# Optimization experiments

Measured on AMD Instinct MI355X. Metric: run time of the kernel, lower is better.

## Reference

```python
import jax, jax.numpy as jnp
import numpy as np

B, T, C = 16, 1024, 1024
H = 4          # wshare
K = 31         # kernel_size


def setup_inputs() -> dict:
    key = jax.random.key(0)
    ks = jax.random.split(key, 8)
    s = 1.0 / np.sqrt(C)
    return {
        "query": jax.random.normal(ks[0], (B, T, C), jnp.float32),
        "key_t": jax.random.normal(ks[1], (B, T, C), jnp.float32),   # unused, API compat
        "value": jax.random.normal(ks[2], (B, T, C), jnp.float32),   # unused, API compat
        "mask": jnp.ones((B, 1, T), jnp.int32),
        "W1": jax.random.uniform(ks[3], (2 * C, C), jnp.float32, -s, s),
        "b1": jnp.zeros((2 * C,), jnp.float32),
        "W2": jax.random.uniform(ks[4], (C, C), jnp.float32, -s, s),
        "b2": jnp.zeros((C,), jnp.float32),
        "conv_w": jax.random.uniform(ks[5], (H, K), jnp.float32, 0.0, 1.0),
        "bias": jnp.zeros((C,), jnp.float32),
    }


def reference(query, key_t, value, mask, W1, b1, W2, b2, conv_w, bias):
    # linear1 + GLU: (B,T,C) -> (B,T,2C) -> (B,T,C)
    x = query @ W1.T + b1
    a, g = jnp.split(x, 2, axis=-1)
    x = a * jax.nn.sigmoid(g)
    # (B,T,C) -> (B,C,T) -> (B*C/H, H, T); channel c uses shared kernel c % H
    x = jnp.transpose(x, (0, 2, 1)).reshape(B * C // H, H, T)
    # softmax-normalized shared kernels (H,K); dropout_rate=0 (eval)
    w = jax.nn.softmax(conv_w, axis=-1)
    y = jax.lax.conv_general_dilated(
        x, w[:, None, :], window_strides=(1,), padding=[(K // 2, K // 2)],
        feature_group_count=H, dimension_numbers=("NCH", "OIH", "NCH"))
    x = y.reshape(B, C, T) + bias[None, :, None]
    x = jnp.transpose(x, (0, 2, 1))               # (B,T,C)
    # padding mask: (B,1,T) -> transpose(-1,-2) -> (B,T,1), zero masked frames
    m = jnp.transpose(mask, (0, 2, 1))
    x = jnp.where(m == 0, 0.0, x)
    return x @ W2.T + b2
```

## Files before the change

### kernel.cpp

```cpp
#include <hip/hip_runtime.h>

typedef __attribute__((ext_vector_type(8))) __bf16 bf16x8;
typedef __attribute__((ext_vector_type(4))) __bf16 bf16x4;
typedef __attribute__((ext_vector_type(4))) float  f32x4;
typedef __attribute__((ext_vector_type(4))) float  float4v;

#define DEV static __device__ __forceinline__

DEV void gload_lds16(const void* g, void* l) {
  __builtin_amdgcn_global_load_lds(
      (const __attribute__((address_space(1))) void*)g,
      (__attribute__((address_space(3))) void*)l, 16, 0, 0);
}

__global__ void cvt_bf16_kernel(const float* __restrict__ in,
                                __bf16* __restrict__ out, int n4) {
  int stride = gridDim.x * blockDim.x;
  for (int i = blockIdx.x * blockDim.x + threadIdx.x; i < n4; i += stride) {
    float4v v = ((const float4v*)in)[i];
    bf16x4 o;
#pragma unroll
    for (int j = 0; j < 4; ++j) o[j] = (__bf16)v[j];
    ((bf16x4*)out)[i] = o;
  }
}

__global__ void softmax_w_kernel(const float* __restrict__ cw,
                                 float* __restrict__ out) {
  int h = threadIdx.x;
  if (h < 4) {
    float m = cw[h * 31];
#pragma unroll
    for (int k = 1; k < 31; ++k) m = fmaxf(m, cw[h * 31 + k]);
    float e[31];
    float s = 0.f;
#pragma unroll
    for (int k = 0; k < 31; ++k) {
      e[k] = __expf(cw[h * 31 + k] - m);
      s += e[k];
    }
    float inv = 1.f / s;
#pragma unroll
    for (int k = 0; k < 31; ++k) out[h * 31 + k] = e[k] * inv;
  }
}

template <int STORE_BF16>
__global__ __launch_bounds__(512, 2)
void gemm256_kernel(const __bf16* __restrict__ A, const __bf16* __restrict__ Bw,
                    const float* __restrict__ bias, void* __restrict__ Cout,
                    int M, int N, int K, int ntn) {
  __shared__ __align__(16) __bf16 Al[4 * 8192];
  __shared__ __align__(16) __bf16 Bl[4 * 8192];

  const int tid  = threadIdx.x;
  const int lane = tid & 63;
  const int w    = tid >> 6;
  const int wm = w >> 2, wn = w & 3;

  const int nwg = gridDim.x;
  const int cpx = nwg >> 3;
  const int bid = blockIdx.x;
  const int wgid = (bid & 7) * cpx + (bid >> 3);
  const int m0 = (wgid / ntn) * 256;
  const int n0 = (wgid % ntn) * 256;

  const int NT = K >> 6;

  const int srow = lane >> 2;
  const int scol = ((lane & 3) * 8) ^ (((lane >> 5) & 1) * 16);
  const __bf16* __restrict__ Abase = A + (long)m0 * K;
  const __bf16* __restrict__ Bbase = Bw + (long)n0 * K;

  const int l15 = lane & 15;
  const int cb  = ((lane >> 4) * 16) ^ (((lane >> 3) & 1) * 32);
  const int aoff = (wm * 128 + l15) * 64 + cb;
  const int boff = (wn * 64 + l15) * 64 + cb;

  f32x4 acc[8][4];
#pragma unroll
  for (int i = 0; i < 8; ++i)
#pragma unroll
    for (int j = 0; j < 4; ++j) {
      acc[i][j][0] = 0.f; acc[i][j][1] = 0.f;
      acc[i][j][2] = 0.f; acc[i][j][3] = 0.f;
    }
  bf16x8 af[8], bf[4];

#define ADST(c, s) (Al + ((c) * 2 + (s)) * 8192)
#define BDST(c, s) (Bl + ((c) * 2 + (s)) * 8192)
#define AGB(c, s) ((const char*)Al + ((c) * 2 + (s)) * 16384)
#define BGB(c, s) ((const char*)Bl + ((c) * 2 + (s)) * 16384)

#define STAGE(base, ktc, dst)                                               \
  {                                                                         \
    const __bf16* _src = (base) + (long)(w * 16 + srow) * K + (ktc) + scol; \
    gload_lds16(_src, (dst) + w * 512);                                     \
    gload_lds16(_src + (long)128 * K, (dst) + 4096 + w * 512);              \
  }

#define PH_MID()                                          \
  __builtin_amdgcn_s_barrier();                           \
  asm volatile("s_waitcnt lgkmcnt(0)" ::: "memory");      \
  __builtin_amdgcn_sched_barrier(0);                      \
  __builtin_amdgcn_s_setprio(1);

#define PH_END(VM)                                          \
  __builtin_amdgcn_s_setprio(0);                            \
  if (VM) asm volatile("s_waitcnt vmcnt(8)" ::: "memory");  \
  __builtin_amdgcn_s_barrier();

#define RD_A03(G)                                                  \
  _Pragma("unroll") for (int i = 0; i < 4; ++i)                    \
      af[i] = *(const bf16x8*)((G) + aoff + i * 1024);
#define RD_A47(G)                                                  \
  _Pragma("unroll") for (int i = 0; i < 4; ++i)                    \
      af[4 + i] = *(const bf16x8*)((G) + aoff + (4 + i) * 1024);
#define RD_B4(G)                                                   \
  _Pragma("unroll") for (int j = 0; j < 4; ++j)                    \
      bf[j] = *(const bf16x8*)((G) + boff + j * 1024);

#define MM03()                                                                 \
  _Pragma("unroll") for (int i = 0; i < 4; ++i)                                \
  _Pragma("unroll") for (int j = 0; j < 4; ++j)                                \
      acc[i][j] = __builtin_amdgcn_mfma_f32_16x16x32_bf16(af[i], bf[j], acc[i][j], 0, 0, 0);
#define MM47()                                                                 \
  _Pragma("unroll") for (int i = 0; i < 4; ++i)                                \
  _Pragma("unroll") for (int j = 0; j < 4; ++j)                                \
      acc[4 + i][j] = __builtin_amdgcn_mfma_f32_16x16x32_bf16(af[4 + i], bf[j], acc[4 + i][j], 0, 0, 0);

  STAGE(Abase, 0, ADST(0, 0));
  STAGE(Bbase, 0, BDST(0, 0));
  STAGE(Abase, 32, ADST(0, 1));
  STAGE(Bbase, 32, BDST(0, 1));
  STAGE(Abase, 64, ADST(1, 0));
  STAGE(Bbase, 64, BDST(1, 0));
  asm volatile("s_waitcnt vmcnt(8)" ::: "memory");
  __builtin_amdgcn_s_barrier();

#define TILE(tt, CUR)                                                \
  {                                                                  \
    const int k1 = (((tt) + 1 < NT) ? (tt) + 1 : NT - 1) * 64 + 32;  \
    const int k2 = (((tt) + 2 < NT) ? (tt) + 2 : NT - 1) * 64;       \
                                                            \
    RD_A03(AGB(CUR, 0)); RD_B4(BGB(CUR, 0));                         \
    STAGE(Abase, k1, ADST(CUR ^ 1, 1));                              \
    PH_MID(); MM03(); PH_END(0);                                     \
                                                            \
    RD_A47(AGB(CUR, 0));                                             \
    STAGE(Bbase, k1, BDST(CUR ^ 1, 1));                              \
    PH_MID(); MM47(); PH_END(1);                                     \
                                                            \
    RD_A03(AGB(CUR, 1)); RD_B4(BGB(CUR, 1));                         \
    STAGE(Abase, k2, ADST(CUR, 0));                                  \
    PH_MID(); MM03(); PH_END(0);                                     \
                                                            \
    RD_A47(AGB(CUR, 1));                                             \
    STAGE(Bbase, k2, BDST(CUR, 0));                                  \
    PH_MID(); MM47(); PH_END(1);                                     \
  }

#pragma unroll 1
  for (int t2 = 0; t2 < NT; t2 += 2) {
    TILE(t2, 0);
    TILE(t2 + 1, 1);
  }

  asm volatile("s_waitcnt vmcnt(0)" ::: "memory");

  const int crow = (lane >> 4) * 4;
  const int ccol = lane & 15;
#pragma unroll
  for (int i = 0; i < 8; ++i) {
#pragma unroll
    for (int j = 0; j < 4; ++j) {
      const int mrow = m0 + wm * 128 + i * 16 + crow;
      const int ncol = n0 + wn * 64 + j * 16 + ccol;
      const float bv = bias[ncol];
#pragma unroll
      for (int r = 0; r < 4; ++r) {
        float v = acc[i][j][r] + bv;
        if (STORE_BF16)
          ((__bf16*)Cout)[(long)(mrow + r) * N + ncol] = (__bf16)v;
        else
          ((float*)Cout)[(long)(mrow + r) * N + ncol] = v;
      }
    }
  }
#undef TILE
#undef STAGE
#undef PH_MID
#undef PH_END
#undef RD_A03
#undef RD_A47
#undef RD_B4
#undef MM03
#undef MM47
#undef ADST
#undef BDST
#undef AGB
#undef BGB
}

__global__ __launch_bounds__(256, 2)
void glu_conv_kernel(const __bf16* __restrict__ X, const float* __restrict__ Wsm,
                     const float* __restrict__ bias, const int* __restrict__ mask,
                     __bf16* __restrict__ Y) {
  const int b  = blockIdx.z;
  const int t0 = blockIdx.y * 64;
  const int c0 = blockIdx.x * 128;
  __shared__ float sgT[128][128];
  __shared__ float swl[124];
  const int tid = threadIdx.x;
  if (tid < 124) swl[tid] = Wsm[tid];

  for (int i = tid; i < 2048; i += 256) {
    const int ttl = i & 127;
    const int cg  = i >> 7;
    if (ttl < 94) {
      const int t = t0 - 15 + ttl;
      float v[8];
      if (t >= 0 && t < 1024) {
        const __bf16* p = X + ((long)(b * 1024 + t)) * 2048 + c0 + cg * 8;
        bf16x8 a8 = *(const bf16x8*)p;
        bf16x8 g8 = *(const bf16x8*)(p + 1024);
#pragma unroll
        for (int j = 0; j < 8; ++j) {
          float av = (float)a8[j], gv = (float)g8[j];
          v[j] = av / (1.f + __expf(-gv));
        }
      } else {
#pragma unroll
        for (int j = 0; j < 8; ++j) v[j] = 0.f;
      }
      const int q = ttl >> 2, e = ttl & 3;
#pragma unroll
      for (int j = 0; j < 8; ++j) {
        const int c = cg * 8 + j;
        sgT[c][((q ^ ((c & 7) << 2)) << 2) + e] = v[j];
      }
    }
  }
  __syncthreads();

  const int cc = tid & 127;
  const int th = tid >> 7;
  const int c  = c0 + cc;
  const float* wrow = swl + (c & 3) * 31;
  const float bv = bias[c];
  float acc[32];
#pragma unroll
  for (int u = 0; u < 32; ++u) acc[u] = bv;
  const int key = (cc & 7) << 2;
#pragma unroll
  for (int qi = 0; qi < 16; ++qi) {
    const int q = th * 8 + qi;
    const f32x4 w4 = *(const f32x4*)&sgT[cc][(q ^ key) << 2];
#pragma unroll
    for (int j = 0; j < 4; ++j) {
      const int rl = qi * 4 + j;
#pragma unroll
      for (int u = 0; u < 32; ++u) {
        const int k = rl - u;
        if (k >= 0 && k < 31) acc[u] += w4[j] * wrow[k];
      }
    }
  }
  const long yb = (long)b * 1024 * 1024;
#pragma unroll
  for (int u = 0; u < 32; ++u) {
    const int gt = t0 + th * 32 + u;
    float v = acc[u];
    if (mask[b * 1024 + gt] == 0) v = 0.f;
    Y[yb + (long)gt * 1024 + c] = (__bf16)v;
  }
}

extern "C" void kernel_launch(void* const* d_in, const int* in_sizes, int n_in,
                              void* d_out, int out_size, void* d_ws, size_t ws_size,
                              hipStream_t stream) {
  const float* q    = (const float*)d_in[0];
  const int*   mask = (const int*)d_in[3];
  const float* W1   = (const float*)d_in[4];
  const float* b1   = (const float*)d_in[5];
  const float* W2   = (const float*)d_in[6];
  const float* b2   = (const float*)d_in[7];
  const float* cw   = (const float*)d_in[8];
  const float* bias = (const float*)d_in[9];

  char* ws = (char*)d_ws;
  __bf16* q_bf  = (__bf16*)(ws);
  __bf16* w1_bf = (__bf16*)(ws + (32u << 20));
  __bf16* w2_bf = (__bf16*)(ws + (36u << 20));
  float*  swm   = (float*)(ws + (38u << 20));
  __bf16* x1    = (__bf16*)d_out;
  __bf16* y_bf  = q_bf;

  cvt_bf16_kernel<<<2048, 256, 0, stream>>>(q, q_bf, 16 * 1024 * 1024 / 4);
  cvt_bf16_kernel<<<512, 256, 0, stream>>>(W1, w1_bf, 2048 * 1024 / 4);
  cvt_bf16_kernel<<<256, 256, 0, stream>>>(W2, w2_bf, 1024 * 1024 / 4);
  softmax_w_kernel<<<1, 64, 0, stream>>>(cw, swm);

  gemm256_kernel<1><<<512, 512, 0, stream>>>(q_bf, w1_bf, b1, (void*)x1,
                                             16384, 2048, 1024, 8);
  glu_conv_kernel<<<dim3(8, 16, 16), 256, 0, stream>>>(x1, swm, bias, mask, y_bf);
  gemm256_kernel<0><<<256, 512, 0, stream>>>(y_bf, w2_bf, b2, d_out,
                                             16384, 1024, 1024, 4);
}
```

Before: 190.6 us.

## Restructure GEMM LDS staging to full 64-wide K tiles with XOR swizzle

Reworks the bf16 GEMM main loop so each stage loads a full 64-wide K slice, 128-byte rows, into LDS with a new XOR swizzle, replacing the previous two 32-wide half slices. It double-buffers whole K tiles, splits each tile into four MFMA quadrants, and drops the sched_barrier. Fragment reads and the vmcnt waits are rewritten to match. The goal is fewer barriers per K step and less LDS bank conflict, at the cost of shallower prefetch (one tile ahead) and full vmcnt(0) drains.

```diff
diff --git a/kernel.cpp b/kernel.cpp
--- a/kernel.cpp
+++ b/kernel.cpp
@@ -67,15 +67,17 @@
 
   const int NT = K >> 6;
 
-  const int srow = lane >> 2;
-  const int scol = ((lane & 3) * 8) ^ (((lane >> 5) & 1) * 16);
+  const int scolE = ((((tid & 7) * 16) ^ (((tid >> 3) & 7) << 4)) >> 1);
   const __bf16* __restrict__ Abase = A + (long)m0 * K;
   const __bf16* __restrict__ Bbase = Bw + (long)n0 * K;
 
   const int l15 = lane & 15;
-  const int cb  = ((lane >> 4) * 16) ^ (((lane >> 3) & 1) * 32);
-  const int aoff = (wm * 128 + l15) * 64 + cb;
-  const int boff = (wn * 64 + l15) * 64 + cb;
+  const int xk  = (l15 & 7) << 4;
+  const int a0  = l15 * 128 + (((lane >> 4) * 16) ^ xk);
+  const int a1  = l15 * 128 + ((((lane >> 4) * 16) + 64) ^ xk);
+  const int bq  = (wn & 1) * 8192;
+  const int b0  = bq + a0;
+  const int b1  = bq + a1;
 
   f32x4 acc[8][4];
 #pragma unroll
@@ -85,79 +87,74 @@
       acc[i][j][0] = 0.f; acc[i][j][1] = 0.f;
       acc[i][j][2] = 0.f; acc[i][j][3] = 0.f;
     }
-  bf16x8 af[8], bf[4];
-
-#define ADST(c, s) (Al + ((c) * 2 + (s)) * 8192)
-#define BDST(c, s) (Bl + ((c) * 2 + (s)) * 8192)
-#define AGB(c, s) ((const char*)Al + ((c) * 2 + (s)) * 16384)
-#define BGB(c, s) ((const char*)Bl + ((c) * 2 + (s)) * 16384)
-
-#define STAGE(base, ktc, dst)                                               \
-  {                                                                         \
-    const __bf16* _src = (base) + (long)(w * 16 + srow) * K + (ktc) + scol; \
-    gload_lds16(_src, (dst) + w * 512);                                     \
-    gload_lds16(_src + (long)128 * K, (dst) + 4096 + w * 512);              \
-  }
-
-#define PH_MID()                                          \
-  __builtin_amdgcn_s_barrier();                           \
-  asm volatile("s_waitcnt lgkmcnt(0)" ::: "memory");      \
-  __builtin_amdgcn_sched_barrier(0);                      \
+  bf16x8 af[8], bf[8];
+
+#define ADST(p, mh) (Al + ((p) * 2 + (mh)) * 8192)
+#define BDST(p, nh) (Bl + ((p) * 2 + (nh)) * 8192)
+#define AWG(p) ((const char*)Al + ((p) * 2 + wm) * 16384)
+#define BWG(p) ((const char*)Bl + ((p) * 2 + (wn >> 1)) * 16384)
+
+#define STAGEG(base, groff, ktc, dst)                                         \
+  {                                                                           \
+    const __bf16* _s = (base) + (long)((groff) + (tid >> 3)) * K + (ktc) + scolE; \
+    gload_lds16(_s, (dst) + tid * 8);                                         \
+    gload_lds16(_s + (long)64 * K, (dst) + 4096 + tid * 8);                   \
+  }
+
+#define PH_MID()                                     \
+  __builtin_amdgcn_s_barrier();                      \
+  asm volatile("s_waitcnt lgkmcnt(0)" ::: "memory"); \
   __builtin_amdgcn_s_setprio(1);
 
-#define PH_END(VM)                                          \
-  __builtin_amdgcn_s_setprio(0);                            \
-  if (VM) asm volatile("s_waitcnt vmcnt(8)" ::: "memory");  \
+#define PH_END(VM)                                                    \
+  __builtin_amdgcn_s_setprio(0);                                      \
+  if ((VM) == 4) asm volatile("s_waitcnt vmcnt(4)" ::: "memory");     \
+  if ((VM) == 0) asm volatile("s_waitcnt vmcnt(0)" ::: "memory");     \
   __builtin_amdgcn_s_barrier();
 
-#define RD_A03(G)                                                  \
-  _Pragma("unroll") for (int i = 0; i < 4; ++i)                    \
-      af[i] = *(const bf16x8*)((G) + aoff + i * 1024);
-#define RD_A47(G)                                                  \
-  _Pragma("unroll") for (int i = 0; i < 4; ++i)                    \
-      af[4 + i] = *(const bf16x8*)((G) + aoff + (4 + i) * 1024);
-#define RD_B4(G)                                                   \
-  _Pragma("unroll") for (int j = 0; j < 4; ++j)                    \
-      bf[j] = *(const bf16x8*)((G) + boff + j * 1024);
-
-#define MM03()                                                                 \
-  _Pragma("unroll") for (int i = 0; i < 4; ++i)                                \
-  _Pragma("unroll") for (int j = 0; j < 4; ++j)                                \
-      acc[i][j] = __builtin_amdgcn_mfma_f32_16x16x32_bf16(af[i], bf[j], acc[i][j], 0, 0, 0);
-#define MM47()                                                                 \
-  _Pragma("unroll") for (int i = 0; i < 4; ++i)                                \
-  _Pragma("unroll") for (int j = 0; j < 4; ++j)                                \
-      acc[4 + i][j] = __builtin_amdgcn_mfma_f32_16x16x32_bf16(af[4 + i], bf[j], acc[4 + i][j], 0, 0, 0);
-
-  STAGE(Abase, 0, ADST(0, 0));
-  STAGE(Bbase, 0, BDST(0, 0));
-  STAGE(Abase, 32, ADST(0, 1));
-  STAGE(Bbase, 32, BDST(0, 1));
-  STAGE(Abase, 64, ADST(1, 0));
-  STAGE(Bbase, 64, BDST(1, 0));
-  asm volatile("s_waitcnt vmcnt(8)" ::: "memory");
+#define RDA(IB, G)                                                \
+  _Pragma("unroll") for (int i2 = 0; i2 < 4; ++i2) {              \
+    af[i2 * 2 + 0] = *(const bf16x8*)((G) + ((IB) + i2) * 2048 + a0); \
+    af[i2 * 2 + 1] = *(const bf16x8*)((G) + ((IB) + i2) * 2048 + a1); \
+  }
+#define RDB(JB, G)                                                \
+  _Pragma("unroll") for (int j2 = 0; j2 < 2; ++j2) {              \
+    bf[(JB) * 2 + j2 * 2 + 0] = *(const bf16x8*)((G) + ((JB) + j2) * 2048 + b0); \
+    bf[(JB) * 2 + j2 * 2 + 1] = *(const bf16x8*)((G) + ((JB) + j2) * 2048 + b1); \
+  }
+
+#define MMQ(IB, JB)                                                           \
+  _Pragma("unroll") for (int i2 = 0; i2 < 4; ++i2)                            \
+  _Pragma("unroll") for (int j2 = 0; j2 < 2; ++j2)                            \
+  _Pragma("unroll") for (int kk = 0; kk < 2; ++kk)                            \
+      acc[(IB) + i2][(JB) + j2] = __builtin_amdgcn_mfma_f32_16x16x32_bf16(    \
+          af[i2 * 2 + kk], bf[(JB) * 2 + j2 * 2 + kk], acc[(IB) + i2][(JB) + j2], 0, 0, 0);
+
+  STAGEG(Abase, 0,   0, ADST(0, 0));
+  STAGEG(Abase, 128, 0, ADST(0, 1));
+  STAGEG(Bbase, 0,   0, BDST(0, 0));
+  STAGEG(Bbase, 128, 0, BDST(0, 1));
+  asm volatile("s_waitcnt vmcnt(0)" ::: "memory");
   __builtin_amdgcn_s_barrier();
 
-#define TILE(tt, CUR)                                                \
-  {                                                                  \
-    const int k1 = (((tt) + 1 < NT) ? (tt) + 1 : NT - 1) * 64 + 32;  \
-    const int k2 = (((tt) + 2 < NT) ? (tt) + 2 : NT - 1) * 64;       \
-                                                            \
-    RD_A03(AGB(CUR, 0)); RD_B4(BGB(CUR, 0));                         \
-    STAGE(Abase, k1, ADST(CUR ^ 1, 1));                              \
-    PH_MID(); MM03(); PH_END(0);                                     \
-                                                            \
-    RD_A47(AGB(CUR, 0));                                             \
-    STAGE(Bbase, k1, BDST(CUR ^ 1, 1));                              \
-    PH_MID(); MM47(); PH_END(1);                                     \
-                                                            \
-    RD_A03(AGB(CUR, 1)); RD_B4(BGB(CUR, 1));                         \
-    STAGE(Abase, k2, ADST(CUR, 0));                                  \
-    PH_MID(); MM03(); PH_END(0);                                     \
-                                                            \
-    RD_A47(AGB(CUR, 1));                                             \
-    STAGE(Bbase, k2, BDST(CUR, 0));                                  \
-    PH_MID(); MM47(); PH_END(1);                                     \
+#define TILE(tt, CUR)                                        \
+  {                                                          \
+    const int ktn = (((tt) + 1 < NT) ? (tt) + 1 : NT - 1) * 64; \
+                                                    \
+    RDA(0, AWG(CUR)); RDB(0, BWG(CUR));                      \
+    STAGEG(Abase, 0,   ktn, ADST(CUR ^ 1, 0));               \
+    STAGEG(Abase, 128, ktn, ADST(CUR ^ 1, 1));               \
+    PH_MID(); MMQ(0, 0); PH_END(9);                          \
+                                                    \
+    RDB(2, BWG(CUR));                                        \
+    STAGEG(Bbase, 0,   ktn, BDST(CUR ^ 1, 0));               \
+    STAGEG(Bbase, 128, ktn, BDST(CUR ^ 1, 1));               \
+    PH_MID(); MMQ(0, 2); PH_END(9);                          \
+                                                    \
+    RDA(4, AWG(CUR));                                        \
+    PH_MID(); MMQ(4, 0); PH_END(4);                          \
+                                                    \
+    PH_MID(); MMQ(4, 2); PH_END(0);                          \
   }
 
 #pragma unroll 1
@@ -188,18 +185,16 @@
     }
   }
 #undef TILE
-#undef STAGE
+#undef STAGEG
 #undef PH_MID
 #undef PH_END
-#undef RD_A03
-#undef RD_A47
-#undef RD_B4
-#undef MM03
-#undef MM47
+#undef RDA
+#undef RDB
+#undef MMQ
 #undef ADST
 #undef BDST
-#undef AGB
-#undef BGB
+#undef AWG
+#undef BWG
 }
 
 __global__ __launch_bounds__(256, 2)
```

After: 186.1 us. 1.02x faster.
